# Kernel optimization log

Measured on AMD Instinct MI355X. Metric: run time of the kernel, lower is better.

## Reference

```python
import jax, jax.numpy as jnp
import numpy as np

D_MODEL = 4096
N_Q_HEADS = 32
N_KV_HEADS = 8
HEAD_DIM = D_MODEL // N_Q_HEADS  # 128
N_REP = N_Q_HEADS // N_KV_HEADS  # 4
BATCH = 2
SEQ = 2048
ROPE_THETA = 10000.0


def setup_inputs() -> dict:
    key = jax.random.key(0)
    ks = jax.random.split(key, 5)
    scale = 0.02
    x = jax.random.normal(ks[0], (BATCH, SEQ, D_MODEL), dtype=jnp.float32)
    w_q = jax.random.normal(ks[1], (D_MODEL, N_Q_HEADS * HEAD_DIM), dtype=jnp.float32) * scale
    w_k = jax.random.normal(ks[2], (D_MODEL, N_KV_HEADS * HEAD_DIM), dtype=jnp.float32) * scale
    w_v = jax.random.normal(ks[3], (D_MODEL, N_KV_HEADS * HEAD_DIM), dtype=jnp.float32) * scale
    w_o = jax.random.normal(ks[4], (N_Q_HEADS * HEAD_DIM, D_MODEL), dtype=jnp.float32) * scale
    # precompute_theta_pos_freqs: freqs_cis = exp(1j * outer(t, inv_freq))
    inv_freq = 1.0 / (ROPE_THETA ** (jnp.arange(0, HEAD_DIM, 2)[: HEAD_DIM // 2] / HEAD_DIM))
    t = jnp.arange(SEQ, dtype=jnp.float32)
    freqs = jnp.outer(t, inv_freq)  # [S, HEAD_DIM//2]
    freqs_cos = jnp.cos(freqs).astype(jnp.float32)
    freqs_sin = jnp.sin(freqs).astype(jnp.float32)
    # additive causal mask [1,1,S,S]
    causal = jnp.tril(jnp.ones((SEQ, SEQ), dtype=bool))
    mask = jnp.where(causal, 0.0, -1e9).astype(jnp.float32)[None, None]
    return {"x": x, "w_q": w_q, "w_k": w_k, "w_v": w_v, "w_o": w_o,
            "freqs_cos": freqs_cos, "freqs_sin": freqs_sin, "mask": mask}


def _apply_rope(t, cos, sin):
    # t: [B,S,H,D]; cos/sin: [S,D//2]. Complex multiply in real arithmetic:
    # (a + bi) * (c + di) = (ac - bd) + (ad + bc)i
    B, S, H, D = t.shape
    tr = t.reshape(B, S, H, D // 2, 2)
    a, b = tr[..., 0], tr[..., 1]
    c = cos[None, :, None, :]
    s = sin[None, :, None, :]
    out = jnp.stack([a * c - b * s, a * s + b * c], axis=-1)
    return out.reshape(B, S, H, D)


def reference(x, w_q, w_k, w_v, w_o, freqs_cos, freqs_sin, mask):
    B, S, _ = x.shape
    xq = (x @ w_q).reshape(B, S, N_Q_HEADS, HEAD_DIM)
    xk = (x @ w_k).reshape(B, S, N_KV_HEADS, HEAD_DIM)
    xv = (x @ w_v).reshape(B, S, N_KV_HEADS, HEAD_DIM)
    xq = _apply_rope(xq, freqs_cos, freqs_sin)
    xk = _apply_rope(xk, freqs_cos, freqs_sin)
    # repeat_kv (tile+reshape == repeat along head axis)
    keys = jnp.repeat(xk, N_REP, axis=2)    # [B,S,Hq,D]
    values = jnp.repeat(xv, N_REP, axis=2)  # [B,S,Hq,D]
    xq = xq.transpose(0, 2, 1, 3)           # [B,Hq,S,D]
    keys = keys.transpose(0, 2, 1, 3)
    values = values.transpose(0, 2, 1, 3)
    scores = jnp.einsum("bhqd,bhkd->bhqk", xq, keys) / jnp.sqrt(
        jnp.asarray(HEAD_DIM, dtype=xq.dtype))
    scores = scores + mask
    probs = jax.nn.softmax(scores, axis=-1).astype(xq.dtype)
    out = jnp.einsum("bhqk,bhkd->bhqd", probs, values)
    out = out.transpose(0, 2, 1, 3).reshape(B, S, N_Q_HEADS * HEAD_DIM)
    return out @ w_o


if __name__ == "__main__":
    inp = setup_inputs()
    y = reference(**inp)
    print(y.shape, y.dtype)
```

## Files before the change

### kernel.cpp

```cpp
#include <hip/hip_runtime.h>
#include <stdint.h>
#include <stddef.h>


typedef __bf16 bf16x8 __attribute__((ext_vector_type(8)));
typedef float floatx4 __attribute__((ext_vector_type(4)));
typedef unsigned short ushort8v __attribute__((ext_vector_type(8)));
typedef unsigned short ushort4v __attribute__((ext_vector_type(4)));
typedef unsigned short ushort2v __attribute__((ext_vector_type(2)));

#define DEV static __device__ __forceinline__

DEV unsigned short f2bf(float f) {
  union { float f; unsigned u; } v; v.f = f;
  unsigned r = v.u + 0x7fffu + ((v.u >> 16) & 1u);
  return (unsigned short)(r >> 16);
}
DEV float bf2f(unsigned short b) {
  union { unsigned u; float f; } v; v.u = ((unsigned)b) << 16;
  return v.f;
}

DEV void gload_lds16(const void* g, void* lds) {
  __builtin_amdgcn_global_load_lds(
      (__attribute__((address_space(1))) void*)(g),
      (__attribute__((address_space(3))) void*)(lds), 16, 0, 0);
}

__global__ __launch_bounds__(256) void cvt_fp32_bf16(
    const float* __restrict__ in, unsigned short* __restrict__ out, int n4) {
  int i = blockIdx.x * 256 + threadIdx.x;
  if (i >= n4) return;
  float4 v = ((const float4*)in)[i];
  ushort4v w;
  w.x = f2bf(v.x); w.y = f2bf(v.y); w.z = f2bf(v.z); w.w = f2bf(v.w);
  *(ushort4v*)(out + (size_t)i * 4) = w;
}

__global__ __launch_bounds__(256) void transpose_cvt(
    const float* __restrict__ in, unsigned short* __restrict__ out, int K, int N) {
  __shared__ float tile[32][33];
  int k0 = blockIdx.x * 32, n0 = blockIdx.y * 32;
  int tx = threadIdx.x & 31, ty = threadIdx.x >> 5;
  for (int i = 0; i < 32; i += 8)
    tile[ty + i][tx] = in[(size_t)(k0 + ty + i) * N + n0 + tx];
  __syncthreads();
  for (int i = 0; i < 32; i += 8)
    out[(size_t)(n0 + ty + i) * K + k0 + tx] = f2bf(tile[tx][ty + i]);
}

template <int STORE_F32>
__global__ __launch_bounds__(256, 2) void gemm_bt(
    const unsigned short* __restrict__ A, const unsigned short* __restrict__ Bt,
    void* __restrict__ Cp, int M, int N, int K) {
  __shared__ __align__(16) unsigned short a_lds[4096];
  __shared__ __align__(16) unsigned short b_lds[4096];
  const int tid = threadIdx.x;
  const int wave = tid >> 6, lane = tid & 63;
  const int quad = lane >> 4, l16 = lane & 15;
  const int m0 = blockIdx.x * 128, n0 = blockIdx.y * 128;
  const int wm = (wave >> 1) * 64, wn = (wave & 1) * 64;

  const int srow = (lane >> 2);
  const int skq = (lane & 3) ^ ((lane >> 2) & 3);

  floatx4 acc[4][4] = {};

  for (int k0 = 0; k0 < K; k0 += 32) {
    __syncthreads();
    for (int s = 0; s < 2; ++s) {
      int t = wave * 2 + s;
      int row = t * 16 + srow;
      gload_lds16(A + (size_t)(m0 + row) * K + k0 + skq * 8, a_lds + t * 512);
      gload_lds16(Bt + (size_t)(n0 + row) * K + k0 + skq * 8, b_lds + t * 512);
    }
    __syncthreads();
    bf16x8 af[4], bfr[4];
    const int pos = (quad ^ (l16 & 3)) * 8;
    for (int i = 0; i < 4; ++i)
      af[i] = *(const bf16x8*)(a_lds + (wm + i * 16 + l16) * 32 + pos);
    for (int j = 0; j < 4; ++j)
      bfr[j] = *(const bf16x8*)(b_lds + (wn + j * 16 + l16) * 32 + pos);
    for (int i = 0; i < 4; ++i)
      for (int j = 0; j < 4; ++j)
        acc[i][j] =
            __builtin_amdgcn_mfma_f32_16x16x32_bf16(af[i], bfr[j], acc[i][j], 0, 0, 0);
  }

  for (int i = 0; i < 4; ++i)
    for (int j = 0; j < 4; ++j)
      for (int r = 0; r < 4; ++r) {
        int row = m0 + wm + i * 16 + quad * 4 + r;
        int col = n0 + wn + j * 16 + l16;
        float v = acc[i][j][r];
        if (STORE_F32)
          ((float*)Cp)[(size_t)row * N + col] = v;
        else
          ((unsigned short*)Cp)[(size_t)row * N + col] = f2bf(v);
      }
}

__global__ __launch_bounds__(256) void rope_q(
    const unsigned short* __restrict__ qkv, const float* __restrict__ fc,
    const float* __restrict__ fs, unsigned short* __restrict__ Qd) {
  int gid = blockIdx.x * 256 + threadIdx.x;
  int i = gid & 63;
  int h = (gid >> 6) & 31;
  int s = (gid >> 11) & 2047;
  int b = gid >> 22;
  int row = b * 2048 + s;
  ushort2v p = *(const ushort2v*)(qkv + (size_t)row * 6144 + h * 128 + 2 * i);
  float a = bf2f(p.x), bb = bf2f(p.y);
  float c = fc[s * 64 + i], sn = fs[s * 64 + i];
  ushort2v w;
  w.x = f2bf(a * c - bb * sn);
  w.y = f2bf(a * sn + bb * c);
  *(ushort2v*)(Qd + ((((size_t)b * 32 + h) * 2048 + s) * 128 + 2 * i)) = w;
}

__global__ __launch_bounds__(256) void rope_k(
    const unsigned short* __restrict__ qkv, const float* __restrict__ fc,
    const float* __restrict__ fs, unsigned short* __restrict__ Kd) {
  int gid = blockIdx.x * 256 + threadIdx.x;
  int i = gid & 63;
  int kvh = (gid >> 6) & 7;
  int s = (gid >> 9) & 2047;
  int b = gid >> 20;
  int row = b * 2048 + s;
  ushort2v p = *(const ushort2v*)(qkv + (size_t)row * 6144 + 4096 + kvh * 128 + 2 * i);
  float a = bf2f(p.x), bb = bf2f(p.y);
  float c = fc[s * 64 + i], sn = fs[s * 64 + i];
  ushort2v w;
  w.x = f2bf(a * c - bb * sn);
  w.y = f2bf(a * sn + bb * c);
  *(ushort2v*)(Kd + ((((size_t)b * 8 + kvh) * 2048 + s) * 128 + 2 * i)) = w;
}

__global__ __launch_bounds__(256) void vtrans(
    const unsigned short* __restrict__ qkv, unsigned short* __restrict__ Vt) {
  __shared__ unsigned short tile[32][33];
  int bk = blockIdx.z;
  int b = bk >> 3, kvh = bk & 7;
  int s0 = blockIdx.x * 32, d0 = blockIdx.y * 32;
  int tx = threadIdx.x & 31, ty = threadIdx.x >> 5;
  for (int i = 0; i < 32; i += 8)
    tile[ty + i][tx] =
        qkv[(size_t)(b * 2048 + s0 + ty + i) * 6144 + 5120 + kvh * 128 + d0 + tx];
  __syncthreads();
  for (int i = 0; i < 32; i += 8)
    Vt[((size_t)bk * 128 + d0 + ty + i) * 2048 + s0 + tx] = tile[tx][ty + i];
}

__global__ __launch_bounds__(256, 2) void attn_kernel(
    const unsigned short* __restrict__ Q,
    const unsigned short* __restrict__ Kd,
    const unsigned short* __restrict__ Vt,
    unsigned short* __restrict__ O) {
  __shared__ __align__(16) unsigned short k_lds[64][136];
  __shared__ __align__(16) unsigned short v_lds[128][72];
  __shared__ __align__(16) unsigned short p_lds[4][16][72];

  const int tid = threadIdx.x;
  const int wave = tid >> 6, lane = tid & 63;
  const int quad = lane >> 4, l16 = lane & 15;
  const int q0 = blockIdx.x * 64;
  const int h = blockIdx.y;
  const int b = blockIdx.z;
  const int kvh = h >> 2;
  const float scale = 0.08838834764831845f;

  const unsigned short* qrow =
      Q + (((size_t)b * 32 + h) * 2048 + q0 + wave * 16 + l16) * 128;
  bf16x8 qf[4];
  for (int t = 0; t < 4; ++t)
    qf[t] = *(const bf16x8*)(qrow + t * 32 + quad * 8);

  float m_i[4], l_i[4];
  for (int r = 0; r < 4; ++r) { m_i[r] = -3.0e38f; l_i[r] = 0.f; }
  floatx4 o_acc[8] = {};

  const unsigned short* kbase = Kd + ((size_t)b * 8 + kvh) * 2048 * 128;
  const unsigned short* vbase = Vt + ((size_t)b * 8 + kvh) * 128 * 2048;

  for (int kb = 0; kb <= q0; kb += 64) {
    __syncthreads();
    for (int s = 0; s < 4; ++s) {
      int g = s * 256 + tid;
      int key = g >> 4, dq = g & 15;
      *(ushort8v*)&k_lds[key][dq * 8] =
          *(const ushort8v*)(kbase + (size_t)(kb + key) * 128 + dq * 8);
    }
    for (int s = 0; s < 4; ++s) {
      int g = s * 256 + tid;
      int d = g >> 3, sq = g & 7;
      *(ushort8v*)&v_lds[d][sq * 8] =
          *(const ushort8v*)(vbase + (size_t)d * 2048 + kb + sq * 8);
    }
    __syncthreads();

    float sv[4][4];
    for (int kt = 0; kt < 4; ++kt) {
      floatx4 a = {0.f, 0.f, 0.f, 0.f};
      for (int t = 0; t < 4; ++t) {
        bf16x8 kf = *(const bf16x8*)&k_lds[kt * 16 + l16][t * 32 + quad * 8];
        a = __builtin_amdgcn_mfma_f32_16x16x32_bf16(qf[t], kf, a, 0, 0, 0);
      }
      for (int r = 0; r < 4; ++r) sv[kt][r] = a[r] * scale;
    }
    if (kb == q0) {
      for (int kt = 0; kt < 4; ++kt) {
        int kcol = kb + kt * 16 + l16;
        for (int r = 0; r < 4; ++r) {
          int qg = q0 + wave * 16 + quad * 4 + r;
          if (kcol > qg) sv[kt][r] -= 1.0e9f;
        }
      }
    }
    float mnew[4], alpha[4];
    for (int r = 0; r < 4; ++r) {
      float mx = fmaxf(fmaxf(sv[0][r], sv[1][r]), fmaxf(sv[2][r], sv[3][r]));
      for (int off = 1; off < 16; off <<= 1)
        mx = fmaxf(mx, __shfl_xor(mx, off));
      mnew[r] = fmaxf(m_i[r], mx);
      alpha[r] = __expf(m_i[r] - mnew[r]);
      m_i[r] = mnew[r];
    }
    for (int r = 0; r < 4; ++r) {
      float sum = 0.f;
      for (int kt = 0; kt < 4; ++kt) {
        float p = __expf(sv[kt][r] - mnew[r]);
        sv[kt][r] = p;
        sum += p;
      }
      for (int off = 1; off < 16; off <<= 1)
        sum += __shfl_xor(sum, off);
      l_i[r] = l_i[r] * alpha[r] + sum;
    }
    for (int nb = 0; nb < 8; ++nb)
      for (int r = 0; r < 4; ++r) o_acc[nb][r] *= alpha[r];
    for (int kt = 0; kt < 4; ++kt)
      for (int r = 0; r < 4; ++r)
        p_lds[wave][quad * 4 + r][kt * 16 + l16] = f2bf(sv[kt][r]);
    __syncthreads();
    for (int tk = 0; tk < 2; ++tk) {
      bf16x8 pa = *(const bf16x8*)&p_lds[wave][l16][tk * 32 + quad * 8];
      for (int nb = 0; nb < 8; ++nb) {
        bf16x8 vb = *(const bf16x8*)&v_lds[nb * 16 + l16][tk * 32 + quad * 8];
        o_acc[nb] = __builtin_amdgcn_mfma_f32_16x16x32_bf16(pa, vb, o_acc[nb], 0, 0, 0);
      }
    }
  }

  for (int nb = 0; nb < 8; ++nb)
    for (int r = 0; r < 4; ++r) {
      int row = b * 2048 + q0 + wave * 16 + quad * 4 + r;
      int col = h * 128 + nb * 16 + l16;
      O[(size_t)row * 4096 + col] = f2bf(o_acc[nb][r] / l_i[r]);
    }
}

extern "C" void kernel_launch(void* const* d_in, const int* in_sizes, int n_in,
                              void* d_out, int out_size, void* d_ws, size_t ws_size,
                              hipStream_t stream) {
  const float* x   = (const float*)d_in[0];
  const float* w_q = (const float*)d_in[1];
  const float* w_k = (const float*)d_in[2];
  const float* w_v = (const float*)d_in[3];
  const float* w_o = (const float*)d_in[4];
  const float* fc  = (const float*)d_in[5];
  const float* fs  = (const float*)d_in[6];
  (void)in_sizes; (void)n_in; (void)out_size; (void)ws_size;

  char* ws = (char*)d_ws;
  unsigned short* xb  = (unsigned short*)(ws);
  unsigned short* wT  = (unsigned short*)(ws + 33554432ull);
  unsigned short* qkv = (unsigned short*)(ws + 83886080ull);
  unsigned short* Kd  = (unsigned short*)(ws + 134217728ull);
  unsigned short* Vt  = (unsigned short*)(ws + 142606336ull);
  unsigned short* Qd  = xb;
  unsigned short* woT = wT;
  unsigned short* Ob  = qkv;

  cvt_fp32_bf16<<<16384, 256, 0, stream>>>(x, xb, 4194304);
  transpose_cvt<<<dim3(128, 128), 256, 0, stream>>>(w_q, wT, 4096, 4096);
  transpose_cvt<<<dim3(128, 32), 256, 0, stream>>>(w_k, wT + (size_t)4096 * 4096, 4096, 1024);
  transpose_cvt<<<dim3(128, 32), 256, 0, stream>>>(w_v, wT + (size_t)5120 * 4096, 4096, 1024);
  gemm_bt<0><<<dim3(32, 48), 256, 0, stream>>>(xb, wT, qkv, 4096, 6144, 4096);
  transpose_cvt<<<dim3(128, 128), 256, 0, stream>>>(w_o, woT, 4096, 4096);
  rope_q<<<32768, 256, 0, stream>>>(qkv, fc, fs, Qd);
  rope_k<<<8192, 256, 0, stream>>>(qkv, fc, fs, Kd);
  vtrans<<<dim3(64, 4, 16), 256, 0, stream>>>(qkv, Vt);
  attn_kernel<<<dim3(32, 32, 2), 256, 0, stream>>>(Qd, Kd, Vt, Ob);
  gemm_bt<1><<<dim3(32, 32), 256, 0, stream>>>(Ob, woT, d_out, 4096, 4096, 4096);
}
```

Measured before the change: 974.5 us.

## Enlarge attention tiles, prefetch K/V via registers, lazy softmax rescale

The attention kernel now uses 512 threads covering 128 query rows per block, so each K/V tile loaded into LDS is shared by twice as many waves. The next K/V tile is prefetched into registers while the current one is computed, hiding global load latency. Waves whose rows are fully masked skip the block, and the online-softmax rescale runs only when the row max grows by more than a threshold. The per-wave P-buffer barrier is removed because each wave reads only its own P slice. Risks are register pressure under the 512,4 launch bound and fewer blocks in flight.

```diff
diff --git a/kernel.cpp b/kernel.cpp
--- a/kernel.cpp
+++ b/kernel.cpp
@@ -151,19 +151,19 @@
     Vt[((size_t)bk * 128 + d0 + ty + i) * 2048 + s0 + tx] = tile[tx][ty + i];
 }
 
-__global__ __launch_bounds__(256, 2) void attn_kernel(
+__global__ __launch_bounds__(512, 4) void attn_kernel(
     const unsigned short* __restrict__ Q,
     const unsigned short* __restrict__ Kd,
     const unsigned short* __restrict__ Vt,
     unsigned short* __restrict__ O) {
   __shared__ __align__(16) unsigned short k_lds[64][136];
   __shared__ __align__(16) unsigned short v_lds[128][72];
-  __shared__ __align__(16) unsigned short p_lds[4][16][72];
+  __shared__ __align__(16) unsigned short p_lds[8][16][72];
 
   const int tid = threadIdx.x;
   const int wave = tid >> 6, lane = tid & 63;
   const int quad = lane >> 4, l16 = lane & 15;
-  const int q0 = blockIdx.x * 64;
+  const int q0 = blockIdx.x * 128;
   const int h = blockIdx.y;
   const int b = blockIdx.z;
   const int kvh = h >> 2;
@@ -182,21 +182,31 @@
   const unsigned short* kbase = Kd + ((size_t)b * 8 + kvh) * 2048 * 128;
   const unsigned short* vbase = Vt + ((size_t)b * 8 + kvh) * 128 * 2048;
 
-  for (int kb = 0; kb <= q0; kb += 64) {
+  const int kk = tid >> 4, kd = tid & 15;
+  const int vd = tid >> 3, vs = tid & 7;
+
+  ushort8v krg[2], vrg[2];
+  krg[0] = *(const ushort8v*)(kbase + (size_t)kk * 128 + kd * 8);
+  krg[1] = *(const ushort8v*)(kbase + (size_t)(kk + 32) * 128 + kd * 8);
+  vrg[0] = *(const ushort8v*)(vbase + (size_t)vd * 2048 + vs * 8);
+  vrg[1] = *(const ushort8v*)(vbase + (size_t)(vd + 64) * 2048 + vs * 8);
+
+  const int kb_last = q0 + 64;
+  for (int kb = 0; kb <= kb_last; kb += 64) {
     __syncthreads();
-    for (int s = 0; s < 4; ++s) {
-      int g = s * 256 + tid;
-      int key = g >> 4, dq = g & 15;
-      *(ushort8v*)&k_lds[key][dq * 8] =
-          *(const ushort8v*)(kbase + (size_t)(kb + key) * 128 + dq * 8);
-    }
-    for (int s = 0; s < 4; ++s) {
-      int g = s * 256 + tid;
-      int d = g >> 3, sq = g & 7;
-      *(ushort8v*)&v_lds[d][sq * 8] =
-          *(const ushort8v*)(vbase + (size_t)d * 2048 + kb + sq * 8);
-    }
+    *(ushort8v*)&k_lds[kk][kd * 8] = krg[0];
+    *(ushort8v*)&k_lds[kk + 32][kd * 8] = krg[1];
+    *(ushort8v*)&v_lds[vd][vs * 8] = vrg[0];
+    *(ushort8v*)&v_lds[vd + 64][vs * 8] = vrg[1];
     __syncthreads();
+    if (kb < kb_last) {
+      int nkb = kb + 64;
+      krg[0] = *(const ushort8v*)(kbase + (size_t)(nkb + kk) * 128 + kd * 8);
+      krg[1] = *(const ushort8v*)(kbase + (size_t)(nkb + kk + 32) * 128 + kd * 8);
+      vrg[0] = *(const ushort8v*)(vbase + (size_t)vd * 2048 + nkb + vs * 8);
+      vrg[1] = *(const ushort8v*)(vbase + (size_t)(vd + 64) * 2048 + nkb + vs * 8);
+    }
+    if (kb > q0 + wave * 16 + 15) continue;
 
     float sv[4][4];
     for (int kt = 0; kt < 4; ++kt) {
@@ -207,7 +217,7 @@
       }
       for (int r = 0; r < 4; ++r) sv[kt][r] = a[r] * scale;
     }
-    if (kb == q0) {
+    if (kb + 63 > q0 + wave * 16) {
       for (int kt = 0; kt < 4; ++kt) {
         int kcol = kb + kt * 16 + l16;
         for (int r = 0; r < 4; ++r) {
@@ -216,32 +226,38 @@
         }
       }
     }
-    float mnew[4], alpha[4];
+    float mx[4];
     for (int r = 0; r < 4; ++r) {
-      float mx = fmaxf(fmaxf(sv[0][r], sv[1][r]), fmaxf(sv[2][r], sv[3][r]));
+      float m = fmaxf(fmaxf(sv[0][r], sv[1][r]), fmaxf(sv[2][r], sv[3][r]));
       for (int off = 1; off < 16; off <<= 1)
-        mx = fmaxf(mx, __shfl_xor(mx, off));
-      mnew[r] = fmaxf(m_i[r], mx);
-      alpha[r] = __expf(m_i[r] - mnew[r]);
-      m_i[r] = mnew[r];
+        m = fmaxf(m, __shfl_xor(m, off));
+      mx[r] = m;
+    }
+    bool grow = false;
+    for (int r = 0; r < 4; ++r) grow |= (mx[r] > m_i[r] + 8.f);
+    if (__any(grow)) {
+      for (int r = 0; r < 4; ++r) {
+        float mnew = fmaxf(m_i[r], mx[r]);
+        float alpha = __expf(m_i[r] - mnew);
+        m_i[r] = mnew;
+        l_i[r] *= alpha;
+        for (int nb = 0; nb < 8; ++nb) o_acc[nb][r] *= alpha;
+      }
     }
     for (int r = 0; r < 4; ++r) {
       float sum = 0.f;
       for (int kt = 0; kt < 4; ++kt) {
-        float p = __expf(sv[kt][r] - mnew[r]);
+        float p = __expf(sv[kt][r] - m_i[r]);
         sv[kt][r] = p;
         sum += p;
       }
       for (int off = 1; off < 16; off <<= 1)
         sum += __shfl_xor(sum, off);
-      l_i[r] = l_i[r] * alpha[r] + sum;
-    }
-    for (int nb = 0; nb < 8; ++nb)
-      for (int r = 0; r < 4; ++r) o_acc[nb][r] *= alpha[r];
+      l_i[r] += sum;
+    }
     for (int kt = 0; kt < 4; ++kt)
       for (int r = 0; r < 4; ++r)
         p_lds[wave][quad * 4 + r][kt * 16 + l16] = f2bf(sv[kt][r]);
-    __syncthreads();
     for (int tk = 0; tk < 2; ++tk) {
       bf16x8 pa = *(const bf16x8*)&p_lds[wave][l16][tk * 32 + quad * 8];
       for (int nb = 0; nb < 8; ++nb) {
@@ -290,6 +306,6 @@
   rope_q<<<32768, 256, 0, stream>>>(qkv, fc, fs, Qd);
   rope_k<<<8192, 256, 0, stream>>>(qkv, fc, fs, Kd);
   vtrans<<<dim3(64, 4, 16), 256, 0, stream>>>(qkv, Vt);
-  attn_kernel<<<dim3(32, 32, 2), 256, 0, stream>>>(Qd, Kd, Vt, Ob);
+  attn_kernel<<<dim3(16, 32, 2), 512, 0, stream>>>(Qd, Kd, Vt, Ob);
   gemm_bt<1><<<dim3(32, 32), 256, 0, stream>>>(Ob, woT, d_out, 4096, 4096, 4096);
 }
```

Result: faster. 932.3 us (-4.3%).
